# Performance work log

Hardware: AMD Instinct MI355X
Metric: run time of the kernel (lower is better)

## Reference

```python
import jax, jax.numpy as jnp
import numpy as np


def setup_inputs() -> dict:
    key = jax.random.key(0)
    k0, k1, k2, k3 = jax.random.split(key, 4)
    B, S, E, D, L = 4, 128, 768, 128, 40
    return {
        "emb0": jax.random.normal(k0, (B, S, E), jnp.float32),
        "emb1": jax.random.normal(k1, (B, S, E), jnp.float32),
        "att": jnp.ones((B, S), dtype=bool),
        "W_arc": jax.random.normal(k2, (D, E), jnp.float32) * 0.05,
        "W_lbl": jax.random.normal(k3, (L, 2 * E), jnp.float32) * 0.05,
    }


def reference(emb0, emb1, att, W_arc, W_lbl):
    B, S, E = emb1.shape
    L = W_lbl.shape[0]
    # --- RootedGraphPredictor: linear transform + all-pairs squared distances ---
    dep = jnp.einsum('bse,de->bsd', emb0, W_arc)                      # [B,S,D]
    diff = dep[:, :, None, :] - dep[:, None, :, :]                    # [B,S,S,D]
    distances = jnp.sum(diff * diff, axis=-1)                         # [B,S,S]
    # log(softmin(distances)) == log_softmax(-distances)
    parent = jax.nn.log_softmax(-distances, axis=-1)                  # [B,S,S]
    # --- DependencyLabelClassifier ---
    # Faithful packing order of emb_sentences_expanded: first S*(S-1) rows are
    # (i,j) pairs in row-major order SKIPPING the diagonal, last S rows are
    # (emb[i], ones). The attention mask, however, is laid out in FULL row-major
    # (j,k) order (index j*S+k) -- this mismatch is in the original code and is
    # reproduced faithfully here.
    p = jnp.arange(S * S)
    tail = p >= S * (S - 1)
    i_comp = p // (S - 1)
    j_raw = p % (S - 1)
    j_comp = j_raw + (j_raw >= i_comp).astype(j_raw.dtype)
    i_idx = jnp.where(tail, p - S * (S - 1), i_comp)
    j_idx = jnp.where(tail, 0, j_comp)
    first = emb1[:, i_idx, :]                                          # [B,S*S,E]
    second = jnp.where(tail[None, :, None], 1.0, emb1[:, j_idx, :])    # [B,S*S,E]
    pair = jnp.concatenate([first, second], axis=-1)                   # [B,S*S,2E]
    mlp_out = jnp.einsum('bpe,le->bpl', pair, W_lbl)                   # [B,S*S,L]
    eye = jnp.eye(S, dtype=bool)
    mask = (att[:, :, None] & att[:, None, :] & ~eye).reshape(B, S * S)
    logits = jnp.where(mask[:, :, None], mlp_out, -jnp.inf)            # [B,S*S,L]
    lbl_logits = jnp.log(logits).reshape(B, S, S, L)                   # log of logits (nan where <=0/-inf)
    lbl_parent = jnp.nan_to_num(lbl_logits + parent[:, :, :, None], nan=-10.0)
    return (dep, distances, lbl_parent)
```

## Files before the change

### kernel.cpp

```cpp
#include <hip/hip_runtime.h>


__device__ __forceinline__ double wsum_f64(double v) {
#pragma unroll
    for (int off = 32; off; off >>= 1) v += __shfl_down(v, off, 64);
    return v;
}

__global__ __launch_bounds__(256) void k1_proj(
    const float* __restrict__ emb0,
    const float* __restrict__ emb1,
    const float* __restrict__ W_arc,
    const float* __restrict__ W_lbl,
    float* __restrict__ out_dep,
    double* __restrict__ A1,
    double* __restrict__ A2,
    double* __restrict__ Cd)
{
    const int tid  = threadIdx.x;
    const int lane = tid & 63;
    const int wv   = tid >> 6;
    const int blk  = blockIdx.x;
    const int base = lane * 4;

    if (blk < 256) {
        __shared__ float e0[1536];
        __shared__ float pd[2 * 128 * 17];
        const int r0 = blk * 2;
        const float* src = emb0 + r0 * 768;
        for (int idx = tid * 4; idx < 1536; idx += 1024)
            *(float4*)(e0 + idx) = *(const float4*)(src + idx);
        __syncthreads();

        const float4 ea0 = *(const float4*)(e0 + base);
        const float4 ea1 = *(const float4*)(e0 + 256 + base);
        const float4 ea2 = *(const float4*)(e0 + 512 + base);
        const float4 eb0 = *(const float4*)(e0 + 768 + base);
        const float4 eb1 = *(const float4*)(e0 + 1024 + base);
        const float4 eb2 = *(const float4*)(e0 + 1280 + base);

        for (int cc = 0; cc < 32; ++cc) {
            const int c = wv * 32 + cc;
            const float* w = W_arc + c * 768 + base;
            const float4 w0 = *(const float4*)(w);
            const float4 w1 = *(const float4*)(w + 256);
            const float4 w2 = *(const float4*)(w + 512);
            float p0 = w0.x*ea0.x + w0.y*ea0.y + w0.z*ea0.z + w0.w*ea0.w
                     + w1.x*ea1.x + w1.y*ea1.y + w1.z*ea1.z + w1.w*ea1.w
                     + w2.x*ea2.x + w2.y*ea2.y + w2.z*ea2.z + w2.w*ea2.w;
            float p1 = w0.x*eb0.x + w0.y*eb0.y + w0.z*eb0.z + w0.w*eb0.w
                     + w1.x*eb1.x + w1.y*eb1.y + w1.z*eb1.z + w1.w*eb1.w
                     + w2.x*eb2.x + w2.y*eb2.y + w2.z*eb2.z + w2.w*eb2.w;
            p0 += __shfl_xor(p0, 16, 64);  p0 += __shfl_xor(p0, 32, 64);
            p1 += __shfl_xor(p1, 16, 64);  p1 += __shfl_xor(p1, 32, 64);
            if (lane < 16) {
                pd[c * 17 + lane]            = p0;
                pd[128 * 17 + c * 17 + lane] = p1;
            }
        }
        __syncthreads();
        {
            const int row = tid >> 7, col = tid & 127;
            const float* p = pd + row * (128 * 17) + col * 17;
            float s = 0.f;
#pragma unroll
            for (int q = 0; q < 16; ++q) s += p[q];
            out_dep[(r0 + row) * 128 + col] = s;
        }
    } else if (blk < 768) {
        __shared__ float e1[768];
        const int row = blk - 256;
        const float* src = emb1 + row * 768;
        if (tid * 4 < 768)
            *(float4*)(e1 + tid * 4) = *(const float4*)(src + tid * 4);
        __syncthreads();

        const float4 fa0 = *(const float4*)(e1 + base);
        const float4 fa1 = *(const float4*)(e1 + 256 + base);
        const float4 fa2 = *(const float4*)(e1 + 512 + base);

        int col = wv * 20;
        const float* w = W_lbl + (col % 40) * 1536 + (col / 40) * 768 + base;
        float4 w0 = *(const float4*)(w);
        float4 w1 = *(const float4*)(w + 256);
        float4 w2 = *(const float4*)(w + 512);
        for (int cc = 0; cc < 20; ++cc) {
            float4 n0, n1, n2;
            if (cc < 19) {
                const int nc = col + 1;
                const float* nw = W_lbl + (nc % 40) * 1536 + (nc / 40) * 768 + base;
                n0 = *(const float4*)(nw);
                n1 = *(const float4*)(nw + 256);
                n2 = *(const float4*)(nw + 512);
            }
            double s = (double)w0.x*fa0.x + (double)w0.y*fa0.y + (double)w0.z*fa0.z + (double)w0.w*fa0.w
                     + (double)w1.x*fa1.x + (double)w1.y*fa1.y + (double)w1.z*fa1.z + (double)w1.w*fa1.w
                     + (double)w2.x*fa2.x + (double)w2.y*fa2.y + (double)w2.z*fa2.z + (double)w2.w*fa2.w;
            s = wsum_f64(s);
            if (lane == 0) {
                const int half = col / 40, l = col - half * 40;
                (half ? A2 : A1)[row * 40 + l] = s;
            }
            col += 1;
            w0 = n0; w1 = n1; w2 = n2;
        }
    } else {
        for (int cc = 0; cc < 10; ++cc) {
            const int l = wv * 10 + cc;
            const float* w = W_lbl + l * 1536 + 768 + base;
            const float4 w0 = *(const float4*)(w);
            const float4 w1 = *(const float4*)(w + 256);
            const float4 w2 = *(const float4*)(w + 512);
            double s = (double)w0.x + (double)w0.y + (double)w0.z + (double)w0.w
                     + (double)w1.x + (double)w1.y + (double)w1.z + (double)w1.w
                     + (double)w2.x + (double)w2.y + (double)w2.z + (double)w2.w;
            s = wsum_f64(s);
            if (lane == 0) Cd[l] = s;
        }
    }
}

__global__ __launch_bounds__(256) void k2_rows(
    const float* __restrict__ dep,
    const double* __restrict__ A1,
    const double* __restrict__ A2,
    const double* __restrict__ Cd,
    float* __restrict__ out_dist,
    float* __restrict__ out_lbl)
{
    __shared__ float depi[128];
    __shared__ float dists[128];
    __shared__ float red[2];
    __shared__ float lse_sh;

    const int tid = threadIdx.x;
    const int bi = blockIdx.x;
    const int b = bi >> 7;
    const int i = bi & 127;
    const float* depb = dep + b * (128 * 128);

    if (tid < 128) depi[tid] = depb[i * 128 + tid];
    __syncthreads();

    float ex = 0.0f;
    if (tid < 128) {
        const int j = tid;
        const float* dj = depb + j * 128;
        float acc = 0.0f;
        for (int d = 0; d < 128; d += 4) {
            float4 v = *(const float4*)(dj + d);
            float d0 = v.x - depi[d + 0];
            float d1 = v.y - depi[d + 1];
            float d2 = v.z - depi[d + 2];
            float d3 = v.w - depi[d + 3];
            acc += d0 * d0 + d1 * d1 + d2 * d2 + d3 * d3;
        }
        dists[j] = acc;
        out_dist[bi * 128 + j] = acc;
        ex = expf(-acc);
    }

    float sum = ex;
#pragma unroll
    for (int off = 32; off >= 1; off >>= 1) sum += __shfl_down(sum, off, 64);
    if (tid < 128 && (tid & 63) == 0) red[tid >> 6] = sum;
    __syncthreads();
    if (tid == 0) lse_sh = logf(red[0] + red[1]);
    __syncthreads();

    const float lse = lse_sh;
    const bool last = (i == 127);
    const double* A1b = A1 + b * (128 * 40);
    const double* A2b = A2 + b * (128 * 40);
    float* outrow = out_lbl + bi * 5120;

    if (!last) {
        const double* a1row0 = A1b + i * 40;
        const double* a1row1 = A1b + (i + 1) * 40;
        for (int k = 0; k < 5; ++k) {
            const int idx = k * 1024 + tid * 4;
            float4 o;
            float* oc = &o.x;
#pragma unroll
            for (int e = 0; e < 4; ++e) {
                const int id = idx + e;
                const int j = id / 40;
                const int l = id - j * 40;
                float r;
                if (j == i) {
                    r = -10.0f;
                } else {
                    const int s2 = i + j;
                    const int carry = (s2 >= 127) ? 1 : 0;
                    const int jr = s2 - 127 * carry;
                    const int jm = jr + ((jr >= i + carry) ? 1 : 0);
                    const double v = (carry ? a1row1[l] : a1row0[l]) + A2b[jm * 40 + l];
                    r = (v > 0.0) ? (logf((float)v) - dists[j] - lse)
                      : ((v < 0.0) ? -10.0f : -3.4028234663852886e+38f);
                }
                oc[e] = r;
            }
            *(float4*)(outrow + idx) = o;
        }
    } else {
        for (int k = 0; k < 5; ++k) {
            const int idx = k * 1024 + tid * 4;
            float4 o;
            float* oc = &o.x;
#pragma unroll
            for (int e = 0; e < 4; ++e) {
                const int id = idx + e;
                const int j = id / 40;
                const int l = id - j * 40;
                float r;
                if (j == i) {
                    r = -10.0f;
                } else {
                    const double v = A1b[j * 40 + l] + Cd[l];
                    r = (v > 0.0) ? (logf((float)v) - dists[j] - lse)
                      : ((v < 0.0) ? -10.0f : -3.4028234663852886e+38f);
                }
                oc[e] = r;
            }
            *(float4*)(outrow + idx) = o;
        }
    }
}

extern "C" void kernel_launch(void* const* d_in, const int* in_sizes, int n_in,
                              void* d_out, int out_size, void* d_ws, size_t ws_size,
                              hipStream_t stream)
{
    const float* emb0  = (const float*)d_in[0];
    const float* emb1  = (const float*)d_in[1];
    const float* W_arc = (const float*)d_in[3];
    const float* W_lbl = (const float*)d_in[4];

    float* out      = (float*)d_out;
    float* out_dep  = out;
    float* out_dist = out + 65536;
    float* out_lbl  = out + 131072;

    char* ws = (char*)d_ws;
    double* A1 = (double*)(ws);
    double* A2 = (double*)(ws + 163840);
    double* Cd = (double*)(ws + 327680);

    hipLaunchKernelGGL(k1_proj, dim3(769), dim3(256), 0, stream,
                       emb0, emb1, W_arc, W_lbl, out_dep, A1, A2, Cd);
    hipLaunchKernelGGL(k2_rows, dim3(512), dim3(256), 0, stream,
                       out_dep, A1, A2, Cd, out_dist, out_lbl);
}
```

Measured before the change: 93.65 us.

## Split projection kernel work across more blocks for higher parallelism

The projection kernel's blocks are subdivided: each emb0 row-pair block now computes 16 of the 128 output columns (8x more blocks), and each emb1 row block computes 20 of the 80 label columns (4x more blocks). This raises the grid from 769 to 4097 blocks, so more of the GPU's compute units are busy during the serial per-block dot product loops. The cost is that each block reloads its input row into shared memory, so there is redundant global traffic and extra block scheduling overhead. The software prefetch of the next weight row is dropped in favor of unrolled loops.

```diff
diff --git a/kernel.cpp b/kernel.cpp
--- a/kernel.cpp
+++ b/kernel.cpp
@@ -23,10 +23,12 @@
     const int blk  = blockIdx.x;
     const int base = lane * 4;
 
-    if (blk < 256) {
+    if (blk < 2048) {
         __shared__ float e0[1536];
-        __shared__ float pd[2 * 128 * 17];
-        const int r0 = blk * 2;
+        __shared__ float pd[2 * 16 * 17];
+        const int r2 = blk >> 3;
+        const int q  = blk & 7;
+        const int r0 = r2 * 2;
         const float* src = emb0 + r0 * 768;
         for (int idx = tid * 4; idx < 1536; idx += 1024)
             *(float4*)(e0 + idx) = *(const float4*)(src + idx);
@@ -39,8 +41,10 @@
         const float4 eb1 = *(const float4*)(e0 + 1024 + base);
         const float4 eb2 = *(const float4*)(e0 + 1280 + base);
 
-        for (int cc = 0; cc < 32; ++cc) {
-            const int c = wv * 32 + cc;
+#pragma unroll
+        for (int cc = 0; cc < 4; ++cc) {
+            const int colloc = wv * 4 + cc;
+            const int c = q * 16 + colloc;
             const float* w = W_arc + c * 768 + base;
             const float4 w0 = *(const float4*)(w);
             const float4 w1 = *(const float4*)(w + 256);
@@ -54,22 +58,24 @@
             p0 += __shfl_xor(p0, 16, 64);  p0 += __shfl_xor(p0, 32, 64);
             p1 += __shfl_xor(p1, 16, 64);  p1 += __shfl_xor(p1, 32, 64);
             if (lane < 16) {
-                pd[c * 17 + lane]            = p0;
-                pd[128 * 17 + c * 17 + lane] = p1;
+                pd[colloc * 17 + lane]           = p0;
+                pd[16 * 17 + colloc * 17 + lane] = p1;
             }
         }
         __syncthreads();
-        {
-            const int row = tid >> 7, col = tid & 127;
-            const float* p = pd + row * (128 * 17) + col * 17;
+        if (tid < 32) {
+            const int row = tid >> 4, colloc = tid & 15;
+            const float* p = pd + row * (16 * 17) + colloc * 17;
             float s = 0.f;
 #pragma unroll
-            for (int q = 0; q < 16; ++q) s += p[q];
-            out_dep[(r0 + row) * 128 + col] = s;
-        }
-    } else if (blk < 768) {
+            for (int qq = 0; qq < 16; ++qq) s += p[qq];
+            out_dep[(r0 + row) * 128 + q * 16 + colloc] = s;
+        }
+    } else if (blk < 4096) {
         __shared__ float e1[768];
-        const int row = blk - 256;
+        const int idx = blk - 2048;
+        const int row = idx >> 2;
+        const int g   = idx & 3;
         const float* src = emb1 + row * 768;
         if (tid * 4 < 768)
             *(float4*)(e1 + tid * 4) = *(const float4*)(src + tid * 4);
@@ -79,30 +85,20 @@
         const float4 fa1 = *(const float4*)(e1 + 256 + base);
         const float4 fa2 = *(const float4*)(e1 + 512 + base);
 
-        int col = wv * 20;
-        const float* w = W_lbl + (col % 40) * 1536 + (col / 40) * 768 + base;
-        float4 w0 = *(const float4*)(w);
-        float4 w1 = *(const float4*)(w + 256);
-        float4 w2 = *(const float4*)(w + 512);
-        for (int cc = 0; cc < 20; ++cc) {
-            float4 n0, n1, n2;
-            if (cc < 19) {
-                const int nc = col + 1;
-                const float* nw = W_lbl + (nc % 40) * 1536 + (nc / 40) * 768 + base;
-                n0 = *(const float4*)(nw);
-                n1 = *(const float4*)(nw + 256);
-                n2 = *(const float4*)(nw + 512);
-            }
+#pragma unroll
+        for (int cc = 0; cc < 5; ++cc) {
+            const int col  = g * 20 + wv * 5 + cc;
+            const int half = col / 40;
+            const int l    = col - half * 40;
+            const float* w = W_lbl + l * 1536 + half * 768 + base;
+            const float4 w0 = *(const float4*)(w);
+            const float4 w1 = *(const float4*)(w + 256);
+            const float4 w2 = *(const float4*)(w + 512);
             double s = (double)w0.x*fa0.x + (double)w0.y*fa0.y + (double)w0.z*fa0.z + (double)w0.w*fa0.w
                      + (double)w1.x*fa1.x + (double)w1.y*fa1.y + (double)w1.z*fa1.z + (double)w1.w*fa1.w
                      + (double)w2.x*fa2.x + (double)w2.y*fa2.y + (double)w2.z*fa2.z + (double)w2.w*fa2.w;
             s = wsum_f64(s);
-            if (lane == 0) {
-                const int half = col / 40, l = col - half * 40;
-                (half ? A2 : A1)[row * 40 + l] = s;
-            }
-            col += 1;
-            w0 = n0; w1 = n1; w2 = n2;
+            if (lane == 0) (half ? A2 : A1)[row * 40 + l] = s;
         }
     } else {
         for (int cc = 0; cc < 10; ++cc) {
@@ -246,7 +242,7 @@
     double* A2 = (double*)(ws + 163840);
     double* Cd = (double*)(ws + 327680);
 
-    hipLaunchKernelGGL(k1_proj, dim3(769), dim3(256), 0, stream,
+    hipLaunchKernelGGL(k1_proj, dim3(4097), dim3(256), 0, stream,
                        emb0, emb1, W_arc, W_lbl, out_dep, A1, A2, Cd);
     hipLaunchKernelGGL(k2_rows, dim3(512), dim3(256), 0, stream,
                        out_dep, A1, A2, Cd, out_dist, out_lbl);
```

Result: no change. 93.29 us (median of 2 runs) (-0.4%).
